# Kernel optimization log

Measured on AMD Instinct MI355X. Metric: run time of the kernel, lower is better.

The kernel has to match this reference:

```python
import jax, jax.numpy as jnp
import numpy as np

N = 100000
F = 128
H = 16
C = 40
E = 3200000


def _gcn_norm(edge_index, num_nodes):
    # add self-loops, compute symmetric normalization (PyG GCNConv default)
    loops = jnp.arange(num_nodes, dtype=edge_index.dtype)
    src = jnp.concatenate([edge_index[0], loops])
    dst = jnp.concatenate([edge_index[1], loops])
    ones = jnp.ones(src.shape[0], dtype=jnp.float32)
    deg = jax.ops.segment_sum(ones, dst, num_segments=num_nodes)
    dinv = jnp.where(deg > 0, jax.lax.rsqrt(deg), 0.0)
    norm = dinv[src] * dinv[dst]  # [E+N]
    return src, dst, norm


def _gcn_conv(x, W, b, src, dst, norm, num_nodes):
    h = x @ W                                   # [N, out] transform first (PyG order)
    msg = h[src] * norm[:, None]                # gather + scale
    agg = jax.ops.segment_sum(msg, dst, num_segments=num_nodes)  # scatter-add
    return agg + b


def setup_inputs() -> dict:
    key = jax.random.key(0)
    k = jax.random.split(key, 6)
    x = jax.random.normal(k[0], (N, F), dtype=jnp.float32)
    edge_index = jax.random.randint(k[1], (2, E), 0, N, dtype=jnp.int64)
    W1 = jax.random.normal(k[2], (F, H), dtype=jnp.float32) / np.sqrt(F)
    b1 = jnp.zeros((H,), dtype=jnp.float32)
    W2 = jax.random.normal(k[3], (H, C), dtype=jnp.float32) / np.sqrt(H)
    b2 = jnp.zeros((C,), dtype=jnp.float32)
    return {"x": x, "edge_index": edge_index, "W1": W1, "b1": b1, "W2": W2, "b2": b2}


def reference(x, edge_index, W1, b1, W2, b2):
    src, dst, norm = _gcn_norm(edge_index, N)
    h = _gcn_conv(x, W1, b1, src, dst, norm, N)
    h = jax.nn.relu(h)
    out = _gcn_conv(h, W2, b2, src, dst, norm, N)
    return out
```

## Files before the change

kernel.cpp:

```cpp
#include <hip/hip_runtime.h>
#include <hip/hip_fp16.h>


#define N_NODES 100000
#define F_IN    128
#define H_MID   16
#define C_OUT   40
#define N_EDGES 3200000

#define EC      8192
#define EBLK    391
#define NBUK    391
#define M_HIST  (NBUK * EBLK)
#define NPART   299
#define SRC_MASK 0x1FFFF
#define NSTRIDE 100352
#define CAP_H   5632


__global__ void __launch_bounds__(1024) k_hist(
    const int* __restrict__ dst, int* __restrict__ hist) {
    __shared__ int h[NBUK];
    int t = threadIdx.x, blk = blockIdx.x;
    for (int i = t; i < NBUK; i += 1024) h[i] = 0;
    __syncthreads();
#pragma unroll
    for (int i = 0; i < EC / 1024; ++i) {
        int e = blk * EC + i * 1024 + t;
        if (e < N_EDGES) atomicAdd(&h[__builtin_nontemporal_load(dst + e) >> 8], 1);
    }
    __syncthreads();
    for (int b = t; b < NBUK; b += 1024) hist[b * EBLK + blk] = h[b];
}

__global__ void __launch_bounds__(512) k_scanA(int* __restrict__ hist,
                                               int* __restrict__ part) {
    __shared__ int s[512];
    int t = threadIdx.x;
    int i = blockIdx.x * 512 + t;
    int v = (i < M_HIST) ? hist[i] : 0;
    s[t] = v;
    __syncthreads();
    for (int off = 1; off < 512; off <<= 1) {
        int x = (t >= off) ? s[t - off] : 0;
        __syncthreads();
        s[t] += x;
        __syncthreads();
    }
    if (i < M_HIST) hist[i] = s[t] - v;
    if (t == 511) part[blockIdx.x] = s[511];
}

__global__ void __launch_bounds__(512) k_scanB(int* __restrict__ part) {
    __shared__ int s[512];
    int t = threadIdx.x;
    int v = (t < NPART) ? part[t] : 0;
    s[t] = v;
    __syncthreads();
    for (int off = 1; off < 512; off <<= 1) {
        int x = (t >= off) ? s[t - off] : 0;
        __syncthreads();
        s[t] += x;
        __syncthreads();
    }
    if (t < NPART) part[t] = s[t] - v;
}

__global__ void __launch_bounds__(1024) k_part(
    const int* __restrict__ src, const int* __restrict__ dst,
    const int* __restrict__ hist, const int* __restrict__ part,
    int* __restrict__ eb) {
    __shared__ int cnt[NBUK];
    __shared__ int scn[512];
    __shared__ int dlt[NBUK];
    __shared__ int cr[NBUK];
    __shared__ int sval[EC];
    __shared__ int spos[EC];
    int t = threadIdx.x, blk = blockIdx.x;
    for (int b = t; b < NBUK; b += 1024) cnt[b] = 0;
    __syncthreads();
    int e0 = blk * EC;
    int d[8], s[8], bk[8];
    bool val[8];
#pragma unroll
    for (int k = 0; k < 8; ++k) {
        int e = e0 + k * 1024 + t;
        val[k] = (e < N_EDGES);
        d[k] = val[k] ? __builtin_nontemporal_load(dst + e) : 0;
        s[k] = val[k] ? __builtin_nontemporal_load(src + e) : 0;
        bk[k] = d[k] >> 8;
    }
#pragma unroll
    for (int k = 0; k < 8; ++k)
        if (val[k]) atomicAdd(&cnt[bk[k]], 1);
    __syncthreads();
    if (t < 512) scn[t] = (t < NBUK) ? cnt[t] : 0;
    __syncthreads();
    for (int off = 1; off < 512; off <<= 1) {
        int x = 0;
        if (t < 512 && t >= off) x = scn[t - off];
        __syncthreads();
        if (t < 512) scn[t] += x;
        __syncthreads();
    }
    for (int b = t; b < NBUK; b += 1024) {
        int idx = b * EBLK + blk;
        int gb = hist[idx] + part[idx >> 9];
        int lb = scn[b] - cnt[b];
        dlt[b] = gb - lb;
        cr[b] = lb;
    }
    __syncthreads();
#pragma unroll
    for (int k = 0; k < 8; ++k) {
        if (val[k]) {
            int lr = atomicAdd(&cr[bk[k]], 1);
            sval[lr] = ((d[k] & 255) << 17) | s[k];
            spos[lr] = lr + dlt[bk[k]];
        }
    }
    __syncthreads();
    int n = (e0 + EC <= N_EDGES) ? EC : (N_EDGES - e0);
    for (int i = t; i < n; i += 1024)
        eb[spos[i]] = sval[i];
}

__global__ void __launch_bounds__(512) k_degrp(
    const int* __restrict__ hist, const int* __restrict__ part,
    const int* __restrict__ eb, int* __restrict__ rp,
    float* __restrict__ dinv) {
    __shared__ int deg[256], scn[256];
    int b = blockIdx.x, t = threadIdx.x;
    int i0 = b * EBLK;
    int bb = hist[i0] + part[i0 >> 9];
    int bn = (b + 1 < NBUK) ? (hist[i0 + EBLK] + part[(i0 + EBLK) >> 9]) : N_EDGES;
    int ecnt = bn - bb;
    if (t < 256) deg[t] = 0;
    __syncthreads();
    for (int i = t; i < ecnt; i += 512)
        atomicAdd(&deg[__builtin_nontemporal_load(eb + bb + i) >> 17], 1);
    __syncthreads();
    if (t < 256) scn[t] = deg[t];
    __syncthreads();
    for (int off = 1; off < 256; off <<= 1) {
        int x = (t < 256 && t >= off) ? scn[t - off] : 0;
        __syncthreads();
        if (t < 256) scn[t] += x;
        __syncthreads();
    }
    if (t < 256) {
        int ex = scn[t] - deg[t];
        int node = b * 256 + t;
        rp[node] = bb + ex;
        dinv[node] = rsqrtf(1.0f + (float)deg[t]);
    }
}


typedef float f4 __attribute__((ext_vector_type(4)));

__global__ void __launch_bounds__(256) k_gemm1(
    const float* __restrict__ x, const float* __restrict__ W1,
    const float* __restrict__ dinv, __half* __restrict__ h1p) {
    __shared__ float w[F_IN * H_MID];
    __shared__ float xs[16 * 132];
    int t = threadIdx.x;
    for (int i = t; i < F_IN * H_MID; i += 256) w[i] = W1[i];
    int tile = blockIdx.x;
    const f4* xg = (const f4*)(x + (size_t)tile * 16 * F_IN);
    f4* xs4 = (f4*)xs;
    for (int i = t; i < 512; i += 256) {
        int r = i >> 5, c4 = i & 31;
        xs4[r * 33 + c4] = __builtin_nontemporal_load(xg + r * 32 + c4);
    }
    __syncthreads();
    int node = t >> 4, j = t & 15;
    const float* xr = xs + node * 132;
    float acc = 0.f;
#pragma unroll 8
    for (int k = 0; k < F_IN; ++k) acc += xr[k] * w[k * H_MID + j];
    int g = tile * 16 + node;
    h1p[(size_t)g * H_MID + j] = __float2half(acc * dinv[g]);
}

__global__ void __launch_bounds__(1024) k_csrg1(
    const int* __restrict__ hist, const int* __restrict__ part,
    const int* __restrict__ eb, const int* __restrict__ rp,
    const float* __restrict__ dinv, const __half* __restrict__ h1p,
    const float* __restrict__ b1, int* __restrict__ es,
    __half* __restrict__ r1p) {
    __shared__ int base[129];
    __shared__ int cw[128];
    __shared__ int esl[CAP_H];
    int bh = blockIdx.x;
    int b = bh >> 1, hi = bh & 1;
    int t = threadIdx.x;
    int i0 = b * EBLK;
    int bb = hist[i0] + part[i0 >> 9];
    int bn = (b + 1 < NBUK) ? (hist[i0 + EBLK] + part[(i0 + EBLK) >> 9]) : N_EDGES;
    int ecnt = bn - bb;
    int n0 = b * 256 + hi * 128;
    if (t < 128) {
        int lb = rp[n0 + t] - bb;
        base[t] = lb;
        cw[t] = lb;
    }
    if (t == 128) base[128] = hi ? ecnt : (rp[b * 256 + 128] - bb);
    __syncthreads();
    int h0 = base[0];
    int hcnt = base[128] - h0;
    int g = t >> 4, j = t & 15;
    if (hcnt <= CAP_H) {
        for (int i = t; i < ecnt; i += 1024) {
            int v = __builtin_nontemporal_load(eb + bb + i);
            int loc = v >> 17;
            if ((loc >> 7) == hi) {
                int r = atomicAdd(&cw[loc & 127], 1);
                esl[r - h0] = v & SRC_MASK;
            }
        }
        __syncthreads();
        for (int i = t; i < hcnt; i += 1024)
            __builtin_nontemporal_store(esl[i], es + bb + h0 + i);
        for (int nd = g; nd < 128; nd += 64) {
            int node = n0 + nd;
            if (node >= N_NODES) continue;
            float dv = dinv[node];
            int beg = base[nd] - h0, end = base[nd + 1] - h0;
            float acc = __half2float(h1p[(size_t)node * H_MID + j]);
            int e = beg;
            for (; e + 8 <= end; e += 8) {
                int s0 = esl[e],     s1 = esl[e + 1], s2 = esl[e + 2], s3 = esl[e + 3];
                int s4 = esl[e + 4], s5 = esl[e + 5], s6 = esl[e + 6], s7 = esl[e + 7];
                acc += __half2float(h1p[(size_t)s0 * H_MID + j])
                     + __half2float(h1p[(size_t)s1 * H_MID + j])
                     + __half2float(h1p[(size_t)s2 * H_MID + j])
                     + __half2float(h1p[(size_t)s3 * H_MID + j])
                     + __half2float(h1p[(size_t)s4 * H_MID + j])
                     + __half2float(h1p[(size_t)s5 * H_MID + j])
                     + __half2float(h1p[(size_t)s6 * H_MID + j])
                     + __half2float(h1p[(size_t)s7 * H_MID + j]);
            }
            for (; e < end; ++e) acc += __half2float(h1p[(size_t)esl[e] * H_MID + j]);
            float a = dv * acc;
            unsigned short o = __half_as_ushort(__float2half(fmaxf(a + b1[j], 0.f) * dv));
            __builtin_nontemporal_store(o, (unsigned short*)(r1p + (size_t)node * H_MID + j));
        }
    } else {
        for (int i = t; i < ecnt; i += 1024) {
            int v = eb[bb + i];
            int loc = v >> 17;
            if ((loc >> 7) == hi) {
                int r = atomicAdd(&cw[loc & 127], 1);
                es[bb + r] = v & SRC_MASK;
            }
        }
        __threadfence_block();
        __syncthreads();
        for (int nd = g; nd < 128; nd += 64) {
            int node = n0 + nd;
            if (node >= N_NODES) continue;
            float dv = dinv[node];
            int beg = bb + base[nd], end = bb + base[nd + 1];
            float acc = __half2float(h1p[(size_t)node * H_MID + j]);
            for (int e = beg; e < end; ++e)
                acc += __half2float(h1p[(size_t)es[e] * H_MID + j]);
            float a = dv * acc;
            unsigned short o = __half_as_ushort(__float2half(fmaxf(a + b1[j], 0.f) * dv));
            __builtin_nontemporal_store(o, (unsigned short*)(r1p + (size_t)node * H_MID + j));
        }
    }
}

__global__ void __launch_bounds__(256) k_gather2(
    const int* __restrict__ rp, const int* __restrict__ es,
    const float* __restrict__ dinv, const __half* __restrict__ r1p,
    const float* __restrict__ W2, const float* __restrict__ b2,
    float* __restrict__ out) {
    __shared__ float w2[H_MID * C_OUT];
    __shared__ float a2[16 * 17];
    int t = threadIdx.x;
    for (int i = t; i < H_MID * C_OUT; i += 256) w2[i] = W2[i];
    int tile = blockIdx.x;
    int node = tile * 16 + (t >> 4), j = t & 15;
    float dv = dinv[node];
    int beg = rp[node], end = rp[node + 1];
    float acc = __half2float(r1p[(size_t)node * H_MID + j]);
    int e = beg;
    for (; e + 8 <= end; e += 8) {
        int s0 = es[e],     s1 = es[e + 1], s2 = es[e + 2], s3 = es[e + 3];
        int s4 = es[e + 4], s5 = es[e + 5], s6 = es[e + 6], s7 = es[e + 7];
        acc += __half2float(r1p[(size_t)s0 * H_MID + j])
             + __half2float(r1p[(size_t)s1 * H_MID + j])
             + __half2float(r1p[(size_t)s2 * H_MID + j])
             + __half2float(r1p[(size_t)s3 * H_MID + j])
             + __half2float(r1p[(size_t)s4 * H_MID + j])
             + __half2float(r1p[(size_t)s5 * H_MID + j])
             + __half2float(r1p[(size_t)s6 * H_MID + j])
             + __half2float(r1p[(size_t)s7 * H_MID + j]);
    }
    for (; e < end; ++e) acc += __half2float(r1p[(size_t)es[e] * H_MID + j]);
    a2[(t >> 4) * 17 + j] = dv * acc;
    __syncthreads();
    for (int idx = t; idx < 16 * C_OUT; idx += 256) {
        int nd = idx / C_OUT, c = idx - nd * C_OUT;
        float s = b2[c];
#pragma unroll
        for (int jj = 0; jj < H_MID; ++jj) s += a2[nd * 17 + jj] * w2[jj * C_OUT + c];
        __builtin_nontemporal_store(s, &out[((size_t)tile * 16 + nd) * C_OUT + c]);
    }
}

extern "C" void kernel_launch(void* const* d_in, const int* in_sizes, int n_in,
                              void* d_out, int out_size, void* d_ws, size_t ws_size,
                              hipStream_t stream) {
    const float* x  = (const float*)d_in[0];
    const int*   ei = (const int*)d_in[1];
    const float* W1 = (const float*)d_in[2];
    const float* b1 = (const float*)d_in[3];
    const float* W2 = (const float*)d_in[4];
    const float* b2 = (const float*)d_in[5];
    float* out = (float*)d_out;

    const int* src = ei;
    const int* dst = ei + N_EDGES;

    int* rp     = (int*)d_ws;
    float* dinv = (float*)(rp + NSTRIDE);
    int* es     = (int*)(dinv + NSTRIDE);
    __half* h1p = (__half*)(es + N_EDGES);
    __half* r1p = h1p + (size_t)NSTRIDE * H_MID;

    int* eb   = (int*)d_out;
    int* hist = eb + N_EDGES;
    int* part = hist + 153088;

    k_hist <<<EBLK, 1024, 0, stream>>>(dst, hist);
    k_scanA<<<NPART, 512, 0, stream>>>(hist, part);
    k_scanB<<<1, 512, 0, stream>>>(part);
    k_part <<<EBLK, 1024, 0, stream>>>(src, dst, hist, part, eb);
    k_degrp<<<NBUK, 512, 0, stream>>>(hist, part, eb, rp, dinv);
    k_gemm1<<<N_NODES / 16, 256, 0, stream>>>(x, W1, dinv, h1p);
    k_csrg1<<<NBUK * 2, 1024, 0, stream>>>(hist, part, eb, rp, dinv, h1p, b1, es, r1p);
    k_gather2<<<N_NODES / 16, 256, 0, stream>>>(rp, es, dinv, r1p, W2, b2, out);
}
```

Baseline: 236.7 us.

## Halve bucket width and rebuild per-bucket CSR in LDS for both layers

Buckets now cover 128 destination nodes instead of 256, so each CSR block owns a whole bucket and sorts its edges in LDS without the half-bucket filtering pass. The global es array is no longer written. The second layer is replaced by k_csrg2, which rebuilds the same LDS edge list from eb instead of reading es, and then does the 16x40 matmul for 128 nodes per block. This trades a global CSR write and read for a second local sort. It doubles the histogram and scan size, and the overflow fallback path is now a quadratic scan.

```diff
diff --git a/kernel.cpp b/kernel.cpp
--- a/kernel.cpp
+++ b/kernel.cpp
@@ -10,9 +10,9 @@
 
 #define EC      8192
 #define EBLK    391
-#define NBUK    391
+#define NBUK    782
 #define M_HIST  (NBUK * EBLK)
-#define NPART   299
+#define NPART   598
 #define SRC_MASK 0x1FFFF
 #define NSTRIDE 100352
 #define CAP_H   5632
@@ -27,7 +27,7 @@
 #pragma unroll
     for (int i = 0; i < EC / 1024; ++i) {
         int e = blk * EC + i * 1024 + t;
-        if (e < N_EDGES) atomicAdd(&h[__builtin_nontemporal_load(dst + e) >> 8], 1);
+        if (e < N_EDGES) atomicAdd(&h[__builtin_nontemporal_load(dst + e) >> 7], 1);
     }
     __syncthreads();
     for (int b = t; b < NBUK; b += 1024) hist[b * EBLK + blk] = h[b];
@@ -51,13 +51,13 @@
     if (t == 511) part[blockIdx.x] = s[511];
 }
 
-__global__ void __launch_bounds__(512) k_scanB(int* __restrict__ part) {
-    __shared__ int s[512];
+__global__ void __launch_bounds__(1024) k_scanB(int* __restrict__ part) {
+    __shared__ int s[1024];
     int t = threadIdx.x;
     int v = (t < NPART) ? part[t] : 0;
     s[t] = v;
     __syncthreads();
-    for (int off = 1; off < 512; off <<= 1) {
+    for (int off = 1; off < 1024; off <<= 1) {
         int x = (t >= off) ? s[t - off] : 0;
         __syncthreads();
         s[t] += x;
@@ -71,7 +71,7 @@
     const int* __restrict__ hist, const int* __restrict__ part,
     int* __restrict__ eb) {
     __shared__ int cnt[NBUK];
-    __shared__ int scn[512];
+    __shared__ int scn[1024];
     __shared__ int dlt[NBUK];
     __shared__ int cr[NBUK];
     __shared__ int sval[EC];
@@ -88,19 +88,18 @@
         val[k] = (e < N_EDGES);
         d[k] = val[k] ? __builtin_nontemporal_load(dst + e) : 0;
         s[k] = val[k] ? __builtin_nontemporal_load(src + e) : 0;
-        bk[k] = d[k] >> 8;
+        bk[k] = d[k] >> 7;
     }
 #pragma unroll
     for (int k = 0; k < 8; ++k)
         if (val[k]) atomicAdd(&cnt[bk[k]], 1);
     __syncthreads();
-    if (t < 512) scn[t] = (t < NBUK) ? cnt[t] : 0;
-    __syncthreads();
-    for (int off = 1; off < 512; off <<= 1) {
-        int x = 0;
-        if (t < 512 && t >= off) x = scn[t - off];
-        __syncthreads();
-        if (t < 512) scn[t] += x;
+    scn[t] = (t < NBUK) ? cnt[t] : 0;
+    __syncthreads();
+    for (int off = 1; off < 1024; off <<= 1) {
+        int x = (t >= off) ? scn[t - off] : 0;
+        __syncthreads();
+        scn[t] += x;
         __syncthreads();
     }
     for (int b = t; b < NBUK; b += 1024) {
@@ -115,7 +114,7 @@
     for (int k = 0; k < 8; ++k) {
         if (val[k]) {
             int lr = atomicAdd(&cr[bk[k]], 1);
-            sval[lr] = ((d[k] & 255) << 17) | s[k];
+            sval[lr] = ((d[k] & 127) << 17) | s[k];
             spos[lr] = lr + dlt[bk[k]];
         }
     }
@@ -129,28 +128,28 @@
     const int* __restrict__ hist, const int* __restrict__ part,
     const int* __restrict__ eb, int* __restrict__ rp,
     float* __restrict__ dinv) {
-    __shared__ int deg[256], scn[256];
+    __shared__ int deg[128], scn[128];
     int b = blockIdx.x, t = threadIdx.x;
     int i0 = b * EBLK;
     int bb = hist[i0] + part[i0 >> 9];
     int bn = (b + 1 < NBUK) ? (hist[i0 + EBLK] + part[(i0 + EBLK) >> 9]) : N_EDGES;
     int ecnt = bn - bb;
-    if (t < 256) deg[t] = 0;
+    if (t < 128) deg[t] = 0;
     __syncthreads();
     for (int i = t; i < ecnt; i += 512)
         atomicAdd(&deg[__builtin_nontemporal_load(eb + bb + i) >> 17], 1);
     __syncthreads();
-    if (t < 256) scn[t] = deg[t];
-    __syncthreads();
-    for (int off = 1; off < 256; off <<= 1) {
-        int x = (t < 256 && t >= off) ? scn[t - off] : 0;
-        __syncthreads();
-        if (t < 256) scn[t] += x;
-        __syncthreads();
-    }
-    if (t < 256) {
+    if (t < 128) scn[t] = deg[t];
+    __syncthreads();
+    for (int off = 1; off < 128; off <<= 1) {
+        int x = (t < 128 && t >= off) ? scn[t - off] : 0;
+        __syncthreads();
+        if (t < 128) scn[t] += x;
+        __syncthreads();
+    }
+    if (t < 128) {
         int ex = scn[t] - deg[t];
-        int node = b * 256 + t;
+        int node = b * 128 + t;
         rp[node] = bb + ex;
         dinv[node] = rsqrtf(1.0f + (float)deg[t]);
     }
@@ -187,46 +186,36 @@
     const int* __restrict__ hist, const int* __restrict__ part,
     const int* __restrict__ eb, const int* __restrict__ rp,
     const float* __restrict__ dinv, const __half* __restrict__ h1p,
-    const float* __restrict__ b1, int* __restrict__ es,
-    __half* __restrict__ r1p) {
+    const float* __restrict__ b1, __half* __restrict__ r1p) {
     __shared__ int base[129];
     __shared__ int cw[128];
     __shared__ int esl[CAP_H];
-    int bh = blockIdx.x;
-    int b = bh >> 1, hi = bh & 1;
-    int t = threadIdx.x;
+    int b = blockIdx.x, t = threadIdx.x;
     int i0 = b * EBLK;
     int bb = hist[i0] + part[i0 >> 9];
     int bn = (b + 1 < NBUK) ? (hist[i0 + EBLK] + part[(i0 + EBLK) >> 9]) : N_EDGES;
     int ecnt = bn - bb;
-    int n0 = b * 256 + hi * 128;
+    int n0 = b * 128;
     if (t < 128) {
         int lb = rp[n0 + t] - bb;
         base[t] = lb;
         cw[t] = lb;
     }
-    if (t == 128) base[128] = hi ? ecnt : (rp[b * 256 + 128] - bb);
-    __syncthreads();
-    int h0 = base[0];
-    int hcnt = base[128] - h0;
+    if (t == 128) base[128] = ecnt;
+    __syncthreads();
     int g = t >> 4, j = t & 15;
-    if (hcnt <= CAP_H) {
+    if (ecnt <= CAP_H) {
         for (int i = t; i < ecnt; i += 1024) {
             int v = __builtin_nontemporal_load(eb + bb + i);
-            int loc = v >> 17;
-            if ((loc >> 7) == hi) {
-                int r = atomicAdd(&cw[loc & 127], 1);
-                esl[r - h0] = v & SRC_MASK;
-            }
-        }
-        __syncthreads();
-        for (int i = t; i < hcnt; i += 1024)
-            __builtin_nontemporal_store(esl[i], es + bb + h0 + i);
+            int r = atomicAdd(&cw[v >> 17], 1);
+            esl[r] = v & SRC_MASK;
+        }
+        __syncthreads();
         for (int nd = g; nd < 128; nd += 64) {
             int node = n0 + nd;
             if (node >= N_NODES) continue;
             float dv = dinv[node];
-            int beg = base[nd] - h0, end = base[nd + 1] - h0;
+            int beg = base[nd], end = base[nd + 1];
             float acc = __half2float(h1p[(size_t)node * H_MID + j]);
             int e = beg;
             for (; e + 8 <= end; e += 8) {
@@ -247,24 +236,16 @@
             __builtin_nontemporal_store(o, (unsigned short*)(r1p + (size_t)node * H_MID + j));
         }
     } else {
-        for (int i = t; i < ecnt; i += 1024) {
-            int v = eb[bb + i];
-            int loc = v >> 17;
-            if ((loc >> 7) == hi) {
-                int r = atomicAdd(&cw[loc & 127], 1);
-                es[bb + r] = v & SRC_MASK;
-            }
-        }
-        __threadfence_block();
-        __syncthreads();
         for (int nd = g; nd < 128; nd += 64) {
             int node = n0 + nd;
             if (node >= N_NODES) continue;
             float dv = dinv[node];
-            int beg = bb + base[nd], end = bb + base[nd + 1];
             float acc = __half2float(h1p[(size_t)node * H_MID + j]);
-            for (int e = beg; e < end; ++e)
-                acc += __half2float(h1p[(size_t)es[e] * H_MID + j]);
+            for (int i = 0; i < ecnt; ++i) {
+                int v = eb[bb + i];
+                if ((v >> 17) == nd)
+                    acc += __half2float(h1p[(size_t)(v & SRC_MASK) * H_MID + j]);
+            }
             float a = dv * acc;
             unsigned short o = __half_as_ushort(__float2half(fmaxf(a + b1[j], 0.f) * dv));
             __builtin_nontemporal_store(o, (unsigned short*)(r1p + (size_t)node * H_MID + j));
@@ -272,42 +253,85 @@
     }
 }
 
-__global__ void __launch_bounds__(256) k_gather2(
-    const int* __restrict__ rp, const int* __restrict__ es,
+__global__ void __launch_bounds__(1024) k_csrg2(
+    const int* __restrict__ hist, const int* __restrict__ part,
+    const int* __restrict__ eb, const int* __restrict__ rp,
     const float* __restrict__ dinv, const __half* __restrict__ r1p,
     const float* __restrict__ W2, const float* __restrict__ b2,
     float* __restrict__ out) {
+    __shared__ int base[129];
+    __shared__ int cw[128];
+    __shared__ int esl[CAP_H];
+    __shared__ float a2[128 * 17];
     __shared__ float w2[H_MID * C_OUT];
-    __shared__ float a2[16 * 17];
-    int t = threadIdx.x;
-    for (int i = t; i < H_MID * C_OUT; i += 256) w2[i] = W2[i];
-    int tile = blockIdx.x;
-    int node = tile * 16 + (t >> 4), j = t & 15;
-    float dv = dinv[node];
-    int beg = rp[node], end = rp[node + 1];
-    float acc = __half2float(r1p[(size_t)node * H_MID + j]);
-    int e = beg;
-    for (; e + 8 <= end; e += 8) {
-        int s0 = es[e],     s1 = es[e + 1], s2 = es[e + 2], s3 = es[e + 3];
-        int s4 = es[e + 4], s5 = es[e + 5], s6 = es[e + 6], s7 = es[e + 7];
-        acc += __half2float(r1p[(size_t)s0 * H_MID + j])
-             + __half2float(r1p[(size_t)s1 * H_MID + j])
-             + __half2float(r1p[(size_t)s2 * H_MID + j])
-             + __half2float(r1p[(size_t)s3 * H_MID + j])
-             + __half2float(r1p[(size_t)s4 * H_MID + j])
-             + __half2float(r1p[(size_t)s5 * H_MID + j])
-             + __half2float(r1p[(size_t)s6 * H_MID + j])
-             + __half2float(r1p[(size_t)s7 * H_MID + j]);
-    }
-    for (; e < end; ++e) acc += __half2float(r1p[(size_t)es[e] * H_MID + j]);
-    a2[(t >> 4) * 17 + j] = dv * acc;
-    __syncthreads();
-    for (int idx = t; idx < 16 * C_OUT; idx += 256) {
+    __shared__ float b2l[C_OUT];
+    int b = blockIdx.x, t = threadIdx.x;
+    int i0 = b * EBLK;
+    int bb = hist[i0] + part[i0 >> 9];
+    int bn = (b + 1 < NBUK) ? (hist[i0 + EBLK] + part[(i0 + EBLK) >> 9]) : N_EDGES;
+    int ecnt = bn - bb;
+    int n0 = b * 128;
+    if (t < H_MID * C_OUT) w2[t] = W2[t];
+    if (t >= 1024 - C_OUT) b2l[t - (1024 - C_OUT)] = b2[t - (1024 - C_OUT)];
+    if (t < 128) {
+        int lb = rp[n0 + t] - bb;
+        base[t] = lb;
+        cw[t] = lb;
+    }
+    if (t == 128) base[128] = ecnt;
+    __syncthreads();
+    int g = t >> 4, j = t & 15;
+    if (ecnt <= CAP_H) {
+        for (int i = t; i < ecnt; i += 1024) {
+            int v = __builtin_nontemporal_load(eb + bb + i);
+            int r = atomicAdd(&cw[v >> 17], 1);
+            esl[r] = v & SRC_MASK;
+        }
+        __syncthreads();
+        for (int nd = g; nd < 128; nd += 64) {
+            int node = n0 + nd;
+            float dv = (node < N_NODES) ? dinv[node] : 0.f;
+            int beg = base[nd], end = base[nd + 1];
+            float acc = (node < N_NODES) ? __half2float(r1p[(size_t)node * H_MID + j]) : 0.f;
+            int e = beg;
+            for (; e + 8 <= end; e += 8) {
+                int s0 = esl[e],     s1 = esl[e + 1], s2 = esl[e + 2], s3 = esl[e + 3];
+                int s4 = esl[e + 4], s5 = esl[e + 5], s6 = esl[e + 6], s7 = esl[e + 7];
+                acc += __half2float(r1p[(size_t)s0 * H_MID + j])
+                     + __half2float(r1p[(size_t)s1 * H_MID + j])
+                     + __half2float(r1p[(size_t)s2 * H_MID + j])
+                     + __half2float(r1p[(size_t)s3 * H_MID + j])
+                     + __half2float(r1p[(size_t)s4 * H_MID + j])
+                     + __half2float(r1p[(size_t)s5 * H_MID + j])
+                     + __half2float(r1p[(size_t)s6 * H_MID + j])
+                     + __half2float(r1p[(size_t)s7 * H_MID + j]);
+            }
+            for (; e < end; ++e) acc += __half2float(r1p[(size_t)esl[e] * H_MID + j]);
+            a2[nd * 17 + j] = dv * acc;
+        }
+    } else {
+        for (int nd = g; nd < 128; nd += 64) {
+            int node = n0 + nd;
+            float dv = (node < N_NODES) ? dinv[node] : 0.f;
+            float acc = (node < N_NODES) ? __half2float(r1p[(size_t)node * H_MID + j]) : 0.f;
+            for (int i = 0; i < ecnt; ++i) {
+                int v = eb[bb + i];
+                if ((v >> 17) == nd)
+                    acc += __half2float(r1p[(size_t)(v & SRC_MASK) * H_MID + j]);
+            }
+            a2[nd * 17 + j] = dv * acc;
+        }
+    }
+    __syncthreads();
+    for (int idx = t; idx < 128 * C_OUT; idx += 1024) {
         int nd = idx / C_OUT, c = idx - nd * C_OUT;
-        float s = b2[c];
-#pragma unroll
-        for (int jj = 0; jj < H_MID; ++jj) s += a2[nd * 17 + jj] * w2[jj * C_OUT + c];
-        __builtin_nontemporal_store(s, &out[((size_t)tile * 16 + nd) * C_OUT + c]);
+        int node = n0 + nd;
+        if (node < N_NODES) {
+            float s = b2l[c];
+#pragma unroll
+            for (int jj = 0; jj < H_MID; ++jj) s += a2[nd * 17 + jj] * w2[jj * C_OUT + c];
+            __builtin_nontemporal_store(s, &out[(size_t)node * C_OUT + c]);
+        }
     }
 }
 
@@ -327,20 +351,18 @@
 
     int* rp     = (int*)d_ws;
     float* dinv = (float*)(rp + NSTRIDE);
-    int* es     = (int*)(dinv + NSTRIDE);
-    __half* h1p = (__half*)(es + N_EDGES);
+    __half* h1p = (__half*)(dinv + NSTRIDE);
     __half* r1p = h1p + (size_t)NSTRIDE * H_MID;
-
-    int* eb   = (int*)d_out;
-    int* hist = eb + N_EDGES;
-    int* part = hist + 153088;
+    int* eb     = (int*)(r1p + (size_t)NSTRIDE * H_MID);
+    int* hist   = eb + N_EDGES;
+    int* part   = hist + 306176;
 
     k_hist <<<EBLK, 1024, 0, stream>>>(dst, hist);
     k_scanA<<<NPART, 512, 0, stream>>>(hist, part);
-    k_scanB<<<1, 512, 0, stream>>>(part);
+    k_scanB<<<1, 1024, 0, stream>>>(part);
     k_part <<<EBLK, 1024, 0, stream>>>(src, dst, hist, part, eb);
     k_degrp<<<NBUK, 512, 0, stream>>>(hist, part, eb, rp, dinv);
     k_gemm1<<<N_NODES / 16, 256, 0, stream>>>(x, W1, dinv, h1p);
-    k_csrg1<<<NBUK * 2, 1024, 0, stream>>>(hist, part, eb, rp, dinv, h1p, b1, es, r1p);
-    k_gather2<<<N_NODES / 16, 256, 0, stream>>>(rp, es, dinv, r1p, W2, b2, out);
-}
+    k_csrg1<<<NBUK, 1024, 0, stream>>>(hist, part, eb, rp, dinv, h1p, b1, r1p);
+    k_csrg2<<<NBUK, 1024, 0, stream>>>(hist, part, eb, rp, dinv, r1p, W2, b2, out);
+}
```

New measurement: 228.5 us. -3.4%, faster.
